# Kernel tuning notes

Measured on AMD Instinct MI355X. Metric: run time of the kernel, lower is better.

## Reference

```python
import jax, jax.numpy as jnp
import numpy as np
from jax.ops import segment_sum

N = 20000; IN = 256; HID = 256; Z = 64; DEC_H = 64; E = 120000; NEG = 5
BETA = 1.0; LN_EPS = 1e-5; TAU_MIN = 1e-4


def setup_inputs() -> dict:
    rng = np.random.default_rng(0)
    a = rng.integers(0, N, E)
    b = (a + 1 + rng.integers(0, N - 1, E)) % N  # guarantees a != b
    lo, hi = np.minimum(a, b), np.maximum(a, b)
    pos_edge = jnp.asarray(np.stack([lo, hi]), dtype=jnp.int32)          # [2,E], i<j single copy
    edge_index = jnp.asarray(np.stack([np.concatenate([lo, hi]),
                                       np.concatenate([hi, lo])]), dtype=jnp.int32)  # [2,2E] undirected
    neg_edge = jnp.asarray(rng.integers(0, N, (2, NEG * E)), dtype=jnp.int32)
    ks = jax.random.split(jax.random.key(0), 12)
    p = lambda i, shape, s=0.02: (jax.random.normal(ks[i], shape, jnp.float32) * s)
    return dict(
        x=p(0, (N, IN), 1.0), eps=p(1, (N, Z), 1.0),
        edge_index=edge_index, pos_edge=pos_edge, neg_edge=neg_edge,
        W1=p(2, (IN, HID)), b1=jnp.zeros((HID,), jnp.float32),
        g1=jnp.ones((HID,), jnp.float32), bt1=jnp.zeros((HID,), jnp.float32),
        Wmu=p(3, (HID, Z)), bmu=jnp.zeros((Z,), jnp.float32),
        Wlv=p(4, (HID, Z)), blv=jnp.zeros((Z,), jnp.float32),
        Wd1=p(5, (Z, Z)), bd1=jnp.zeros((Z,), jnp.float32),
        Wd2=p(6, (Z, Z)), bd2=jnp.zeros((Z,), jnp.float32),
        Wa=p(7, (4 * Z, DEC_H)), ba=jnp.zeros((DEC_H,), jnp.float32),
        Wb=p(8, (DEC_H, 1)), bb=jnp.zeros((1,), jnp.float32),
        tau=jnp.array(1.0, jnp.float32))


def _gcn_plain(h, src, dst, W, b):
    # GCNConv(add_self_loops=False, normalize=False): unnormalized scatter-add
    m = h @ W                                   # [N,F]
    return segment_sum(m[src], dst, num_segments=N) + b


def _gcn_norm(h, src, dst, W, b):
    # GCNConv defaults: self loops + symmetric normalization
    loops = jnp.arange(N, dtype=src.dtype)
    s = jnp.concatenate([src, loops]); d = jnp.concatenate([dst, loops])
    deg = segment_sum(jnp.ones_like(d, jnp.float32), d, num_segments=N)  # in-degree incl self
    dis = jax.lax.rsqrt(jnp.maximum(deg, 1.0))
    norm = dis[s] * dis[d]                      # [Emsg+N]
    m = h @ W
    return segment_sum(m[s] * norm[:, None], d, num_segments=N) + b


def _layernorm(h, g, bt):
    mu = jnp.mean(h, axis=-1, keepdims=True)
    var = jnp.mean((h - mu) ** 2, axis=-1, keepdims=True)
    return (h - mu) * jax.lax.rsqrt(var + LN_EPS) * g + bt


def _forward(x, eps, edge_index, pos_edge, neg_edge, W1, b1, g1, bt1, Wmu, bmu,
             Wlv, blv, Wd1, bd1, Wd2, bd2, Wa, ba, Wb, bb, tau):
    src, dst = edge_index[0], edge_index[1]
    # Encoder (dropout inactive: eval-mode reference)
    h1 = jax.nn.relu(_layernorm(_gcn_plain(x, src, dst, W1, b1), g1, bt1))
    mu = _gcn_plain(h1, src, dst, Wmu, bmu)
    logvar = _gcn_plain(h1, src, dst, Wlv, blv)
    z = mu + eps * jnp.exp(0.5 * logvar)
    # EdgeDecoder: 2 normalized GCN passes over positive (i<j) edges only
    ps, pd = pos_edge[0], pos_edge[1]
    h = jax.nn.relu(_gcn_norm(z, ps, pd, Wd1, bd1))
    h = jax.nn.relu(_gcn_norm(h, ps, pd, Wd2, bd2))
    # edge gather -> concat features -> MLP
    eu = jnp.concatenate([pos_edge[0], neg_edge[0]])
    ev = jnp.concatenate([pos_edge[1], neg_edge[1]])
    hu, hv = h[eu], h[ev]                        # [Ep+En, Z]
    phi = jnp.concatenate([hu, hv, jnp.abs(hu - hv), hu * hv], axis=-1)  # [Ep+En, 4Z]
    logits = (jax.nn.relu(phi @ Wa + ba) @ Wb + bb)[:, 0]
    logits = logits / jnp.clip(tau, TAU_MIN)
    # weighted BCE-with-logits; pos_weight = #neg/#pos = NEG
    n_pos = pos_edge.shape[1]; n_neg = neg_edge.shape[1]
    labels = jnp.concatenate([jnp.ones((n_pos,), jnp.float32), jnp.zeros((n_neg,), jnp.float32)])
    pw = jnp.float32(n_neg) / jnp.float32(n_pos)
    recon = -jnp.mean(pw * labels * jax.nn.log_sigmoid(logits)
                      + (1.0 - labels) * jax.nn.log_sigmoid(-logits))
    kl = -0.5 * jnp.mean(1.0 + logvar - mu ** 2 - jnp.exp(logvar))
    loss = recon + BETA * kl
    return loss, recon, kl


def reference(x, eps, edge_index, pos_edge, neg_edge, W1, b1, g1, bt1, Wmu, bmu,
              Wlv, blv, Wd1, bd1, Wd2, bd2, Wa, ba, Wb, bb, tau):
    return _forward(x, eps, edge_index, pos_edge, neg_edge, W1, b1, g1, bt1, Wmu,
                    bmu, Wlv, blv, Wd1, bd1, Wd2, bd2, Wa, ba, Wb, bb, tau)
```

## Files before the change

kernel.cpp:

```cpp
#include <hip/hip_runtime.h>
#include <hip/hip_bf16.h>
#include <math.h>

#define N_NODES 20000
#define E2      240000
#define EP      120000
#define ENEG    600000
#define ETOT    720000
#define NTILE   11250
#define EMLP_BLOCKS 1024

#define WA_B  64
#define W1T_B 256
#define WML_B 128
#define UV_B  2813
#define HA_B  938
#define HP_B  469
#define FA_B  938
#define FP_B  469
#define DIS_B 79

typedef __attribute__((ext_vector_type(8))) short bf16x8;
typedef __attribute__((ext_vector_type(4))) float f32x4;

__device__ __forceinline__ float logsigf(float x) {
    return fminf(x, 0.0f) - log1pf(expf(-fabsf(x)));
}

__device__ __forceinline__ unsigned short f2bf(float f) {
    unsigned u = __float_as_uint(f);
    u += 0x7FFF + ((u >> 16) & 1);
    return (unsigned short)(u >> 16);
}

__device__ __forceinline__ float bflo(unsigned u) { return __uint_as_float(u << 16); }
__device__ __forceinline__ float bfhi(unsigned u) { return __uint_as_float(u & 0xFFFF0000u); }

__device__ __forceinline__ void store_out(float v, float* p) { *p = v; }
__device__ __forceinline__ void store_out(float v, unsigned short* p) { *p = f2bf(v); }

__device__ __forceinline__ int4 pack_phi(unsigned hu, unsigned hv) {
    const float fu0 = __uint_as_float(hu << 16);
    const float fu1 = __uint_as_float(hu & 0xFFFF0000u);
    const float fv0 = __uint_as_float(hv << 16);
    const float fv1 = __uint_as_float(hv & 0xFFFF0000u);
    const float ad0 = fabsf(fu0 - fv0), ad1 = fabsf(fu1 - fv1);
    const float pr0 = fu0 * fv0,        pr1 = fu1 * fv1;
    union { __hip_bfloat162 h; int u; } c0, c1;
    c0.h = __float22bfloat162_rn(float2{ad0, pr0});
    c1.h = __float22bfloat162_rn(float2{ad1, pr1});
    int4 r;
    r.x = (int)((hu & 0xFFFFu) | (hv << 16));
    r.y = c0.u;
    r.z = (int)((hu >> 16) | (hv & 0xFFFF0000u));
    r.w = c1.u;
    return r;
}

__global__ void k_prep_csr(const float* __restrict__ Wa, unsigned short* __restrict__ WaT,
                           const float* __restrict__ W1, unsigned short* __restrict__ W1T,
                           const float* __restrict__ Wmu, const float* __restrict__ Wlv,
                           unsigned short* __restrict__ WmlT,
                           const int* __restrict__ pos, const int* __restrict__ neg,
                           int2* __restrict__ uv,
                           const int* __restrict__ e_dst, int* __restrict__ cntA,
                           const int* __restrict__ pd, int* __restrict__ cntP) {
    const int b = blockIdx.x, tid = threadIdx.x;
    if (b < WA_B) {
        const int idx = b * 256 + tid;
        const int n = idx >> 8, kp = idx & 255;
        const int d = kp >> 2, part = kp & 3;
        WaT[idx] = f2bf(Wa[(part * 64 + d) * 64 + n]);
    } else if (b < WA_B + W1T_B) {
        const int idx = (b - WA_B) * 256 + tid;
        const int n = idx >> 8, k = idx & 255;
        W1T[idx] = f2bf(W1[k * 256 + n]);
    } else if (b < WA_B + W1T_B + WML_B) {
        const int idx = (b - WA_B - W1T_B) * 256 + tid;
        const int n = idx >> 8, k = idx & 255;
        const float* W = (n & 1) ? Wlv : Wmu;
        WmlT[idx] = f2bf(W[k * 64 + (n >> 1)]);
    } else if (b < WA_B + W1T_B + WML_B + UV_B) {
        const int j = (b - WA_B - W1T_B - WML_B) * 256 + tid;
        if (j < ETOT) {
            int u, v;
            if (j < EP) { u = pos[j]; v = pos[EP + j]; }
            else        { u = neg[j - EP]; v = neg[ENEG + (j - EP)]; }
            uv[j] = make_int2(u, v);
        }
    } else if (b < WA_B + W1T_B + WML_B + UV_B + HA_B) {
        const int e = (b - WA_B - W1T_B - WML_B - UV_B) * 256 + tid;
        if (e < E2) atomicAdd(&cntA[e_dst[e]], 1);
    } else {
        const int e = (b - WA_B - W1T_B - WML_B - UV_B - HA_B) * 256 + tid;
        if (e < EP) atomicAdd(&cntP[pd[e]], 1);
    }
}

__global__ __launch_bounds__(1024) void k_scan2(int* __restrict__ cntA, int* __restrict__ rsA,
                                                int* __restrict__ cntP, int* __restrict__ rsP) {
    int* cnt = blockIdx.x ? cntP : cntA;
    int* rs  = blockIdx.x ? rsP  : rsA;
    int* cur = cnt;
    const int n = N_NODES;
    __shared__ int wexc[16];
    __shared__ int s_carry, s_tot;
    const int tid = threadIdx.x, lane = tid & 63, wid = tid >> 6;
    if (tid == 0) s_carry = 0;
    __syncthreads();
    for (int base = 0; base < n; base += 1024) {
        const int i = base + tid;
        const int v = (i < n) ? cnt[i] : 0;
        int x = v;
#pragma unroll
        for (int d = 1; d < 64; d <<= 1) {
            const int t = __shfl_up(x, d, 64);
            if (lane >= d) x += t;
        }
        if (lane == 63) wexc[wid] = x;
        __syncthreads();
        if (tid == 0) {
            int a = 0;
#pragma unroll
            for (int k = 0; k < 16; ++k) { const int t = wexc[k]; wexc[k] = a; a += t; }
            s_tot = a;
        }
        __syncthreads();
        const int excl = s_carry + wexc[wid] + x - v;
        if (i < n) { rs[i] = excl; cur[i] = excl; }
        __syncthreads();
        if (tid == 0) s_carry += s_tot;
        __syncthreads();
    }
    if (tid == 0) rs[n] = s_carry;
}

__global__ void k_finish_csr(const int* __restrict__ e_src, const int* __restrict__ e_dst,
                             int* __restrict__ curA, int* __restrict__ adjA,
                             const int* __restrict__ ps, const int* __restrict__ pd,
                             int* __restrict__ curP, int* __restrict__ adjP,
                             const int* __restrict__ rsP, float* __restrict__ dis) {
    const int b = blockIdx.x, tid = threadIdx.x;
    if (b < FA_B) {
        const int e = b * 256 + tid;
        if (e < E2) {
            const int p = atomicAdd(&curA[e_dst[e]], 1);
            adjA[p] = e_src[e];
        }
    } else if (b < FA_B + FP_B) {
        const int e = (b - FA_B) * 256 + tid;
        if (e < EP) {
            const int p = atomicAdd(&curP[pd[e]], 1);
            adjP[p] = ps[e];
        }
    } else {
        const int i = (b - FA_B - FP_B) * 256 + tid;
        if (i < N_NODES) dis[i] = rsqrtf((float)(rsP[i + 1] - rsP[i] + 1));
    }
}

__global__ __launch_bounds__(256) void k_mm_xW1_mfma(const float* __restrict__ x,
                                                     const unsigned short* __restrict__ W1T,
                                                     unsigned short* __restrict__ m1) {
    __shared__ unsigned short sA[32 * 264];
    const int tid = threadIdx.x;
    const int w = tid >> 6, lane = tid & 63;
    const int l15 = lane & 15, quad = lane >> 4;
    const int mb = blockIdx.x >> 2, nb = blockIdx.x & 3;

    for (int i = tid; i < 2048; i += 256) {
        const int row = i >> 6, kc = (i & 63) << 2;
        const float4 xv = *(const float4*)&x[((long)mb * 32 + row) * 256 + kc];
        union { unsigned short s[4]; unsigned long long ll; } pk;
        pk.s[0] = f2bf(xv.x); pk.s[1] = f2bf(xv.y);
        pk.s[2] = f2bf(xv.z); pk.s[3] = f2bf(xv.w);
        *(unsigned long long*)&sA[row * 264 + kc] = pk.ll;
    }

    bf16x8 breg[8];
#pragma unroll
    for (int ks = 0; ks < 8; ++ks)
        breg[ks] = *(const bf16x8*)&W1T[((nb * 64 + w * 16 + l15) << 8) + ks * 32 + quad * 8];
    __syncthreads();

    f32x4 acc[2];
    acc[0] = (f32x4){0.f,0.f,0.f,0.f};
    acc[1] = (f32x4){0.f,0.f,0.f,0.f};
#pragma unroll
    for (int ks = 0; ks < 8; ++ks) {
#pragma unroll
        for (int st = 0; st < 2; ++st) {
            const bf16x8 af = *(const bf16x8*)&sA[(st * 16 + l15) * 264 + ks * 32 + quad * 8];
            acc[st] = __builtin_amdgcn_mfma_f32_16x16x32_bf16(af, breg[ks], acc[st], 0, 0, 0);
        }
    }
#pragma unroll
    for (int st = 0; st < 2; ++st)
#pragma unroll
        for (int r = 0; r < 4; ++r)
            m1[((long)mb * 32 + st * 16 + quad * 4 + r) * 256 + nb * 64 + w * 16 + l15] =
                f2bf(acc[st][r]);
}

__global__ __launch_bounds__(256) void k_gather_ln(const unsigned short* __restrict__ m1,
                                                   const int* __restrict__ rs,
                                                   const int* __restrict__ adj,
                                                   const float* __restrict__ b1,
                                                   const float* __restrict__ g1,
                                                   const float* __restrict__ bt1,
                                                   unsigned short* __restrict__ h1) {
    const int wid = threadIdx.x >> 6, lane = threadIdx.x & 63;
    const int n = blockIdx.x * 4 + wid;
    const int beg = rs[n], end = rs[n + 1];
    float4 a0 = {0.f,0.f,0.f,0.f}, a1 = {0.f,0.f,0.f,0.f};
    int j = beg;
    for (; j + 1 < end; j += 2) {
        const int s0 = adj[j], s1 = adj[j + 1];
        const uint2 u = *(const uint2*)(m1 + (long)s0 * 256 + lane * 4);
        const uint2 v = *(const uint2*)(m1 + (long)s1 * 256 + lane * 4);
        a0.x += bflo(u.x); a0.y += bfhi(u.x); a0.z += bflo(u.y); a0.w += bfhi(u.y);
        a1.x += bflo(v.x); a1.y += bfhi(v.x); a1.z += bflo(v.y); a1.w += bfhi(v.y);
    }
    if (j < end) {
        const int s0 = adj[j];
        const uint2 u = *(const uint2*)(m1 + (long)s0 * 256 + lane * 4);
        a0.x += bflo(u.x); a0.y += bfhi(u.x); a0.z += bflo(u.y); a0.w += bfhi(u.y);
    }
    float4 v;
    const float4 b = *(const float4*)(b1 + lane * 4);
    v.x = a0.x + a1.x + b.x; v.y = a0.y + a1.y + b.y;
    v.z = a0.z + a1.z + b.z; v.w = a0.w + a1.w + b.w;
    float s  = v.x + v.y + v.z + v.w;
    float sq = v.x * v.x + v.y * v.y + v.z * v.z + v.w * v.w;
    for (int o = 32; o > 0; o >>= 1) {
        s  += __shfl_xor(s, o, 64);
        sq += __shfl_xor(sq, o, 64);
    }
    const float mean = s * (1.0f / 256.0f);
    const float var  = sq * (1.0f / 256.0f) - mean * mean;
    const float rsv = rsqrtf(var + 1e-5f);
    const float4 g  = *(const float4*)(g1 + lane * 4);
    const float4 bt = *(const float4*)(bt1 + lane * 4);
    union { unsigned short sh[4]; unsigned long long ll; } pk;
    pk.sh[0] = f2bf(fmaxf((v.x - mean) * rsv * g.x + bt.x, 0.f));
    pk.sh[1] = f2bf(fmaxf((v.y - mean) * rsv * g.y + bt.y, 0.f));
    pk.sh[2] = f2bf(fmaxf((v.z - mean) * rsv * g.z + bt.z, 0.f));
    pk.sh[3] = f2bf(fmaxf((v.w - mean) * rsv * g.w + bt.w, 0.f));
    *(unsigned long long*)&h1[(long)n * 256 + lane * 4] = pk.ll;
}

__global__ __launch_bounds__(256) void k_mm_hml_mfma(const unsigned short* __restrict__ h1,
                                                     const unsigned short* __restrict__ WmlT,
                                                     unsigned short* __restrict__ hml) {
    __shared__ unsigned short sA[32 * 264];
    const int tid = threadIdx.x;
    const int w = tid >> 6, lane = tid & 63;
    const int l15 = lane & 15, quad = lane >> 4;
    const int mb = blockIdx.x >> 1, nb = blockIdx.x & 1;

    for (int i = tid; i < 1024; i += 256) {
        const int row = i >> 5, kc = (i & 31) << 3;
        *(int4*)&sA[row * 264 + kc] = *(const int4*)&h1[((long)mb * 32 + row) * 256 + kc];
    }

    bf16x8 breg[8];
#pragma unroll
    for (int ks = 0; ks < 8; ++ks)
        breg[ks] = *(const bf16x8*)&WmlT[((nb * 64 + w * 16 + l15) << 8) + ks * 32 + quad * 8];
    __syncthreads();

    f32x4 acc[2];
    acc[0] = (f32x4){0.f,0.f,0.f,0.f};
    acc[1] = (f32x4){0.f,0.f,0.f,0.f};
#pragma unroll
    for (int ks = 0; ks < 8; ++ks) {
#pragma unroll
        for (int st = 0; st < 2; ++st) {
            const bf16x8 af = *(const bf16x8*)&sA[(st * 16 + l15) * 264 + ks * 32 + quad * 8];
            acc[st] = __builtin_amdgcn_mfma_f32_16x16x32_bf16(af, breg[ks], acc[st], 0, 0, 0);
        }
    }
#pragma unroll
    for (int st = 0; st < 2; ++st)
#pragma unroll
        for (int r = 0; r < 4; ++r)
            hml[((long)mb * 32 + st * 16 + quad * 4 + r) * 128 + nb * 64 + w * 16 + l15] =
                f2bf(acc[st][r]);
}

__global__ __launch_bounds__(256) void k_gather_mulv(const unsigned short* __restrict__ hml,
                                                     const int* __restrict__ rs,
                                                     const int* __restrict__ adj,
                                                     const float* __restrict__ bmu,
                                                     const float* __restrict__ blv,
                                                     const float* __restrict__ eps,
                                                     float* __restrict__ z,
                                                     double* __restrict__ kl_part) {
    __shared__ double sKL[4];
    const int wid = threadIdx.x >> 6, lane = threadIdx.x & 63;
    const int n = blockIdx.x * 4 + wid;
    const int beg = rs[n], end = rs[n + 1];
    float amu0 = 0.f, amu1 = 0.f, alv0 = 0.f, alv1 = 0.f;
    int j = beg;
    for (; j + 1 < end; j += 2) {
        const int s0 = adj[j], s1 = adj[j + 1];
        const unsigned u0 = *(const unsigned*)(hml + (long)s0 * 128 + lane * 2);
        const unsigned u1 = *(const unsigned*)(hml + (long)s1 * 128 + lane * 2);
        amu0 += bflo(u0); alv0 += bfhi(u0);
        amu1 += bflo(u1); alv1 += bfhi(u1);
    }
    if (j < end) {
        const int s0 = adj[j];
        const unsigned u0 = *(const unsigned*)(hml + (long)s0 * 128 + lane * 2);
        amu0 += bflo(u0); alv0 += bfhi(u0);
    }
    const float mu = amu0 + amu1 + bmu[lane];
    const float lv = alv0 + alv1 + blv[lane];
    z[(long)n * 64 + lane] = mu + eps[(long)n * 64 + lane] * expf(0.5f * lv);
    float term = 1.0f + lv - mu * mu - expf(lv);
    for (int o = 32; o > 0; o >>= 1) term += __shfl_xor(term, o, 64);
    if (lane == 0) sKL[wid] = (double)term;
    __syncthreads();
    if (threadIdx.x == 0)
        kl_part[blockIdx.x] = sKL[0] + sKL[1] + sKL[2] + sKL[3];
}

template <typename OUT>
__global__ __launch_bounds__(256) void k_dec_fused(const float* __restrict__ feat,
                                                   const int* __restrict__ rs,
                                                   const int* __restrict__ adj,
                                                   const float* __restrict__ dis,
                                                   const float* __restrict__ Wd,
                                                   const float* __restrict__ bd,
                                                   OUT* __restrict__ out) {
    __shared__ float sW[64 * 64];
    __shared__ float rows[4][64];
    const int tid = threadIdx.x;
    {
        const float4* w4 = (const float4*)Wd;
        float4* sw4 = (float4*)sW;
        for (int i = tid; i < 1024; i += 256) sw4[i] = w4[i];
    }
    const int wid = tid >> 6, lane = tid & 63;
    const int n = blockIdx.x * 4 + wid;
    const int beg = rs[n], end = rs[n + 1];
    float a0 = 0.f, a1 = 0.f;
    int j = beg;
    for (; j + 1 < end; j += 2) {
        const int s0 = adj[j], s1 = adj[j + 1];
        a0 += feat[(long)s0 * 64 + lane] * dis[s0];
        a1 += feat[(long)s1 * 64 + lane] * dis[s1];
    }
    if (j < end) {
        const int s0 = adj[j];
        a0 += feat[(long)s0 * 64 + lane] * dis[s0];
    }
    const float dn = dis[n];
    rows[wid][lane] = (a0 + a1) * dn + feat[(long)n * 64 + lane] * dn * dn;
    __syncthreads();
    float acc = 0.f;
    for (int k = 0; k < 64; k += 4) {
        const float4 a = *(const float4*)&rows[wid][k];
        acc += a.x * sW[(k+0)*64+lane] + a.y * sW[(k+1)*64+lane]
             + a.z * sW[(k+2)*64+lane] + a.w * sW[(k+3)*64+lane];
    }
    store_out(fmaxf(acc + bd[lane], 0.f), &out[(long)n * 64 + lane]);
}

__global__ __launch_bounds__(256, 4) void k_edge_mlp_mfma(
        const unsigned short* __restrict__ h2bf,
        const int2* __restrict__ uv,
        const unsigned short* __restrict__ WaT,
        const float* __restrict__ ba,
        const float* __restrict__ Wb,
        const float* __restrict__ bb,
        const float* __restrict__ tau,
        double* __restrict__ recon_part) {
    __shared__ unsigned short sPhi[64 * 264];
    __shared__ float sEp[256];
    __shared__ double sRed[4];
    const int tid = threadIdx.x;
    const int w = tid >> 6, lane = tid & 63;
    const int l15 = lane & 15, quad = lane >> 4;
    const int ge = lane >> 3;
    const int c  = lane & 7;

    bf16x8 breg[8];
#pragma unroll
    for (int ks = 0; ks < 8; ++ks)
        breg[ks] = *(const bf16x8*)&WaT[(w * 16 + l15) * 256 + ks * 32 + quad * 8];

    const float4 ba4 = *(const float4*)&ba[w * 16 + quad * 4];
    const float4 wb4 = *(const float4*)&Wb[w * 16 + quad * 4];
    const float bb0 = bb[0];
    const float itau = 1.0f / fmaxf(tau[0], 1e-4f);

    float lsum = 0.f;

    int t = blockIdx.x;
    int2 uv0 = uv[(long)t * 64 + w * 16 + ge];
    int2 uv1 = uv[(long)t * 64 + w * 16 + 8 + ge];
    int4 hu0 = *(const int4*)&h2bf[(long)uv0.x * 64 + c * 8];
    int4 hv0 = *(const int4*)&h2bf[(long)uv0.y * 64 + c * 8];
    int4 hu1 = *(const int4*)&h2bf[(long)uv1.x * 64 + c * 8];
    int4 hv1 = *(const int4*)&h2bf[(long)uv1.y * 64 + c * 8];

    for (; t < NTILE; t += EMLP_BLOCKS) {
        {
            unsigned short* d0 = &sPhi[(w * 16 + ge) * 264 + c * 32];
            *(int4*)(d0 +  0) = pack_phi((unsigned)hu0.x, (unsigned)hv0.x);
            *(int4*)(d0 +  8) = pack_phi((unsigned)hu0.y, (unsigned)hv0.y);
            *(int4*)(d0 + 16) = pack_phi((unsigned)hu0.z, (unsigned)hv0.z);
            *(int4*)(d0 + 24) = pack_phi((unsigned)hu0.w, (unsigned)hv0.w);
            unsigned short* d1 = &sPhi[(w * 16 + 8 + ge) * 264 + c * 32];
            *(int4*)(d1 +  0) = pack_phi((unsigned)hu1.x, (unsigned)hv1.x);
            *(int4*)(d1 +  8) = pack_phi((unsigned)hu1.y, (unsigned)hv1.y);
            *(int4*)(d1 + 16) = pack_phi((unsigned)hu1.z, (unsigned)hv1.z);
            *(int4*)(d1 + 24) = pack_phi((unsigned)hu1.w, (unsigned)hv1.w);
        }
        __syncthreads();

        const int tn = t + EMLP_BLOCKS;
        if (tn < NTILE) {
            uv0 = uv[(long)tn * 64 + w * 16 + ge];
            uv1 = uv[(long)tn * 64 + w * 16 + 8 + ge];
            hu0 = *(const int4*)&h2bf[(long)uv0.x * 64 + c * 8];
            hv0 = *(const int4*)&h2bf[(long)uv0.y * 64 + c * 8];
            hu1 = *(const int4*)&h2bf[(long)uv1.x * 64 + c * 8];
            hv1 = *(const int4*)&h2bf[(long)uv1.y * 64 + c * 8];
        }

        f32x4 acc[4];
#pragma unroll
        for (int mt = 0; mt < 4; ++mt) acc[mt] = (f32x4){0.f, 0.f, 0.f, 0.f};
#pragma unroll
        for (int ks = 0; ks < 8; ++ks) {
#pragma unroll
            for (int mt = 0; mt < 4; ++mt) {
                const bf16x8 bf = *(const bf16x8*)&sPhi[(mt * 16 + l15) * 264 +
                                                        ks * 32 + quad * 8];
                acc[mt] = __builtin_amdgcn_mfma_f32_16x16x32_bf16(breg[ks], bf, acc[mt], 0, 0, 0);
            }
        }

        float sv[4];
#pragma unroll
        for (int mt = 0; mt < 4; ++mt) {
            float s = fmaxf(acc[mt][0] + ba4.x, 0.f) * wb4.x
                    + fmaxf(acc[mt][1] + ba4.y, 0.f) * wb4.y
                    + fmaxf(acc[mt][2] + ba4.z, 0.f) * wb4.z
                    + fmaxf(acc[mt][3] + ba4.w, 0.f) * wb4.w;
            s += __shfl_xor(s, 16, 64);
            s += __shfl_xor(s, 32, 64);
            sv[mt] = s;
        }
        const float ssel = (quad == 0) ? sv[0] : (quad == 1) ? sv[1]
                         : (quad == 2) ? sv[2] : sv[3];
        sEp[(w << 6) + lane] = ssel;
        __syncthreads();

        if (lane < 16) {
            const int et = (w << 4) + lane;
            const float s_e = sEp[et] + sEp[64 + et] + sEp[128 + et] + sEp[192 + et];
            const long j = (long)t * 64 + et;
            const float logit = (s_e + bb0) * itau;
            lsum += (j < EP) ? 5.0f * logsigf(logit) : logsigf(-logit);
        }
    }

    for (int o = 32; o > 0; o >>= 1) lsum += __shfl_xor(lsum, o, 64);
    if (lane == 0) sRed[w] = (double)lsum;
    __syncthreads();
    if (tid == 0)
        recon_part[blockIdx.x] = sRed[0] + sRed[1] + sRed[2] + sRed[3];
}

__global__ __launch_bounds__(1024) void k_final(const double* __restrict__ kl_part,
                                                const double* __restrict__ recon_part,
                                                float* __restrict__ out) {
    __shared__ double sK[16], sR[16];
    const int tid = threadIdx.x, lane = tid & 63, wid = tid >> 6;
    double kl = 0.0, rc = 0.0;
    for (int i = tid; i < 5000; i += 1024) kl += kl_part[i];
    for (int i = tid; i < EMLP_BLOCKS; i += 1024) rc += recon_part[i];
    for (int o = 32; o > 0; o >>= 1) {
        kl += __shfl_xor(kl, o, 64);
        rc += __shfl_xor(rc, o, 64);
    }
    if (lane == 0) { sK[wid] = kl; sR[wid] = rc; }
    __syncthreads();
    if (tid == 0) {
        double K = 0.0, R = 0.0;
        for (int i = 0; i < 16; ++i) { K += sK[i]; R += sR[i]; }
        const double recon = -R / (double)ETOT;
        const double klv = -0.5 * K / ((double)N_NODES * 64.0);
        out[0] = (float)(recon + klv);
        out[1] = (float)recon;
        out[2] = (float)klv;
    }
}

extern "C" void kernel_launch(void* const* d_in, const int* in_sizes, int n_in,
                              void* d_out, int out_size, void* d_ws, size_t ws_size,
                              hipStream_t stream) {
    const float* x   = (const float*)d_in[0];
    const float* eps = (const float*)d_in[1];
    const int* EI    = (const int*)d_in[2];
    const int* pos   = (const int*)d_in[3];
    const int* neg   = (const int*)d_in[4];
    const float* W1  = (const float*)d_in[5];
    const float* b1  = (const float*)d_in[6];
    const float* g1  = (const float*)d_in[7];
    const float* bt1 = (const float*)d_in[8];
    const float* Wmu = (const float*)d_in[9];
    const float* bmu = (const float*)d_in[10];
    const float* Wlv = (const float*)d_in[11];
    const float* blv = (const float*)d_in[12];
    const float* Wd1 = (const float*)d_in[13];
    const float* bd1 = (const float*)d_in[14];
    const float* Wd2 = (const float*)d_in[15];
    const float* bd2 = (const float*)d_in[16];
    const float* Wa  = (const float*)d_in[17];
    const float* ba  = (const float*)d_in[18];
    const float* Wb  = (const float*)d_in[19];
    const float* bb  = (const float*)d_in[20];
    const float* tau = (const float*)d_in[21];

    const int* e_src = EI;
    const int* e_dst = EI + E2;
    const int* ps = pos;
    const int* pd = pos + EP;

    float* ws = (float*)d_ws;
    unsigned short* m1bf  = (unsigned short*)ws;
    unsigned short* hmlbf = (unsigned short*)ws;
    float* hdec  = ws + 2560000;
    unsigned short* h2bf = (unsigned short*)(ws + 3840000);
    unsigned short* h1bf = (unsigned short*)(ws + 5120000);
    float* z     = ws + 10240000;
    float* dis   = ws + 11520000;
    unsigned short* WaT = (unsigned short*)(ws + 11540004);
    int* cntA = (int*)(ws + 11548200);
    int* rsA  = (int*)(ws + 11568200);
    int* adjA = (int*)(ws + 11588204);
    int* cntP = (int*)(ws + 11828204);
    int* rsP  = (int*)(ws + 11848204);
    int* adjP = (int*)(ws + 11868208);
    int2* uv  = (int2*)(ws + 11988208);
    double* kl_part    = (double*)(ws + 13428208);
    double* recon_part = (double*)(ws + 13438208);
    unsigned short* W1T  = (unsigned short*)(ws + 13440256);
    unsigned short* WmlT = (unsigned short*)(ws + 13473024);

    hipMemsetAsync(cntA, 0, N_NODES * 4, stream);
    hipMemsetAsync(cntP, 0, N_NODES * 4, stream);

    k_prep_csr<<<WA_B + W1T_B + WML_B + UV_B + HA_B + HP_B, 256, 0, stream>>>(
        Wa, WaT, W1, W1T, Wmu, Wlv, WmlT, pos, neg, uv, e_dst, cntA, pd, cntP);
    k_scan2<<<2, 1024, 0, stream>>>(cntA, rsA, cntP, rsP);
    k_finish_csr<<<FA_B + FP_B + DIS_B, 256, 0, stream>>>(
        e_src, e_dst, cntA, adjA, ps, pd, cntP, adjP, rsP, dis);

    k_mm_xW1_mfma<<<2500, 256, 0, stream>>>(x, W1T, m1bf);
    k_gather_ln<<<5000, 256, 0, stream>>>(m1bf, rsA, adjA, b1, g1, bt1, h1bf);
    k_mm_hml_mfma<<<1250, 256, 0, stream>>>(h1bf, WmlT, hmlbf);
    k_gather_mulv<<<5000, 256, 0, stream>>>(hmlbf, rsA, adjA, bmu, blv, eps, z, kl_part);

    k_dec_fused<float><<<5000, 256, 0, stream>>>(z, rsP, adjP, dis, Wd1, bd1, hdec);
    k_dec_fused<unsigned short><<<5000, 256, 0, stream>>>(hdec, rsP, adjP, dis, Wd2, bd2, h2bf);

    k_edge_mlp_mfma<<<EMLP_BLOCKS, 256, 0, stream>>>(h2bf, uv, WaT, ba, Wb, bb, tau, recon_part);
    k_final<<<1, 1024, 0, stream>>>(kl_part, recon_part, (float*)d_out);
}
```

Measured before the change: 353.1 us.

## Store decoder intermediates in bf16 and retile edge-MLP MFMA as 2x2 per wave

The latent z and the first decoder hidden layer are now stored as bf16 instead of fp32, which halves the bytes moved by the neighbor gathers in both decoder kernels. The edge-MLP kernel changes its wave split from one 16-column N slice over all 64 edges to a 2x2 (edge half × column half) layout. Each wave now reuses each phi fragment loaded from LDS for two MFMAs, which cuts LDS reads, at the cost of twice as many weight registers. Rounding z and the decoder hidden layer to bf16 adds precision loss.

Result: no change. 358.1 us (+1.4%).

```diff
diff --git a/kernel.cpp b/kernel.cpp
--- a/kernel.cpp
+++ b/kernel.cpp
@@ -38,6 +38,10 @@
 
 __device__ __forceinline__ void store_out(float v, float* p) { *p = v; }
 __device__ __forceinline__ void store_out(float v, unsigned short* p) { *p = f2bf(v); }
+__device__ __forceinline__ float load_in(const float* p) { return *p; }
+__device__ __forceinline__ float load_in(const unsigned short* p) {
+    return __uint_as_float(((unsigned)*p) << 16);
+}
 
 __device__ __forceinline__ int4 pack_phi(unsigned hu, unsigned hv) {
     const float fu0 = __uint_as_float(hu << 16);
@@ -294,7 +298,7 @@
                                                      const float* __restrict__ bmu,
                                                      const float* __restrict__ blv,
                                                      const float* __restrict__ eps,
-                                                     float* __restrict__ z,
+                                                     unsigned short* __restrict__ z,
                                                      double* __restrict__ kl_part) {
     __shared__ double sKL[4];
     const int wid = threadIdx.x >> 6, lane = threadIdx.x & 63;
@@ -316,7 +320,7 @@
     }
     const float mu = amu0 + amu1 + bmu[lane];
     const float lv = alv0 + alv1 + blv[lane];
-    z[(long)n * 64 + lane] = mu + eps[(long)n * 64 + lane] * expf(0.5f * lv);
+    z[(long)n * 64 + lane] = f2bf(mu + eps[(long)n * 64 + lane] * expf(0.5f * lv));
     float term = 1.0f + lv - mu * mu - expf(lv);
     for (int o = 32; o > 0; o >>= 1) term += __shfl_xor(term, o, 64);
     if (lane == 0) sKL[wid] = (double)term;
@@ -325,8 +329,8 @@
         kl_part[blockIdx.x] = sKL[0] + sKL[1] + sKL[2] + sKL[3];
 }
 
-template <typename OUT>
-__global__ __launch_bounds__(256) void k_dec_fused(const float* __restrict__ feat,
+template <typename IN, typename OUT>
+__global__ __launch_bounds__(256) void k_dec_fused(const IN* __restrict__ feat,
                                                    const int* __restrict__ rs,
                                                    const int* __restrict__ adj,
                                                    const float* __restrict__ dis,
@@ -348,15 +352,15 @@
     int j = beg;
     for (; j + 1 < end; j += 2) {
         const int s0 = adj[j], s1 = adj[j + 1];
-        a0 += feat[(long)s0 * 64 + lane] * dis[s0];
-        a1 += feat[(long)s1 * 64 + lane] * dis[s1];
+        a0 += load_in(&feat[(long)s0 * 64 + lane]) * dis[s0];
+        a1 += load_in(&feat[(long)s1 * 64 + lane]) * dis[s1];
     }
     if (j < end) {
         const int s0 = adj[j];
-        a0 += feat[(long)s0 * 64 + lane] * dis[s0];
+        a0 += load_in(&feat[(long)s0 * 64 + lane]) * dis[s0];
     }
     const float dn = dis[n];
-    rows[wid][lane] = (a0 + a1) * dn + feat[(long)n * 64 + lane] * dn * dn;
+    rows[wid][lane] = (a0 + a1) * dn + load_in(&feat[(long)n * 64 + lane]) * dn * dn;
     __syncthreads();
     float acc = 0.f;
     for (int k = 0; k < 64; k += 4) {
@@ -377,21 +381,30 @@
         const float* __restrict__ tau,
         double* __restrict__ recon_part) {
     __shared__ unsigned short sPhi[64 * 264];
-    __shared__ float sEp[256];
+    __shared__ float sEp[128];
     __shared__ double sRed[4];
     const int tid = threadIdx.x;
     const int w = tid >> 6, lane = tid & 63;
     const int l15 = lane & 15, quad = lane >> 4;
     const int ge = lane >> 3;
     const int c  = lane & 7;
-
-    bf16x8 breg[8];
-#pragma unroll
-    for (int ks = 0; ks < 8; ++ks)
-        breg[ks] = *(const bf16x8*)&WaT[(w * 16 + l15) * 256 + ks * 32 + quad * 8];
-
-    const float4 ba4 = *(const float4*)&ba[w * 16 + quad * 4];
-    const float4 wb4 = *(const float4*)&Wb[w * 16 + quad * 4];
+    const int eh = w & 1;
+    const int nh = w >> 1;
+
+    bf16x8 breg[2][8];
+#pragma unroll
+    for (int nt = 0; nt < 2; ++nt)
+#pragma unroll
+        for (int ks = 0; ks < 8; ++ks)
+            breg[nt][ks] = *(const bf16x8*)&WaT[(nh * 32 + nt * 16 + l15) * 256 +
+                                                ks * 32 + quad * 8];
+
+    float4 ba4[2], wb4[2];
+#pragma unroll
+    for (int nt = 0; nt < 2; ++nt) {
+        ba4[nt] = *(const float4*)&ba[nh * 32 + nt * 16 + quad * 4];
+        wb4[nt] = *(const float4*)&Wb[nh * 32 + nt * 16 + quad * 4];
+    }
     const float bb0 = bb[0];
     const float itau = 1.0f / fmaxf(tau[0], 1e-4f);
 
@@ -430,39 +443,46 @@
             hv1 = *(const int4*)&h2bf[(long)uv1.y * 64 + c * 8];
         }
 
-        f32x4 acc[4];
-#pragma unroll
-        for (int mt = 0; mt < 4; ++mt) acc[mt] = (f32x4){0.f, 0.f, 0.f, 0.f};
+        f32x4 acc[2][2];
+#pragma unroll
+        for (int mt = 0; mt < 2; ++mt)
+#pragma unroll
+            for (int nt = 0; nt < 2; ++nt) acc[mt][nt] = (f32x4){0.f, 0.f, 0.f, 0.f};
 #pragma unroll
         for (int ks = 0; ks < 8; ++ks) {
 #pragma unroll
-            for (int mt = 0; mt < 4; ++mt) {
-                const bf16x8 bf = *(const bf16x8*)&sPhi[(mt * 16 + l15) * 264 +
+            for (int mt = 0; mt < 2; ++mt) {
+                const bf16x8 bf = *(const bf16x8*)&sPhi[(eh * 32 + mt * 16 + l15) * 264 +
                                                         ks * 32 + quad * 8];
-                acc[mt] = __builtin_amdgcn_mfma_f32_16x16x32_bf16(breg[ks], bf, acc[mt], 0, 0, 0);
+#pragma unroll
+                for (int nt = 0; nt < 2; ++nt)
+                    acc[mt][nt] = __builtin_amdgcn_mfma_f32_16x16x32_bf16(
+                        breg[nt][ks], bf, acc[mt][nt], 0, 0, 0);
             }
         }
 
-        float sv[4];
-#pragma unroll
-        for (int mt = 0; mt < 4; ++mt) {
-            float s = fmaxf(acc[mt][0] + ba4.x, 0.f) * wb4.x
-                    + fmaxf(acc[mt][1] + ba4.y, 0.f) * wb4.y
-                    + fmaxf(acc[mt][2] + ba4.z, 0.f) * wb4.z
-                    + fmaxf(acc[mt][3] + ba4.w, 0.f) * wb4.w;
+        float sv[2];
+#pragma unroll
+        for (int mt = 0; mt < 2; ++mt) {
+            float s = 0.f;
+#pragma unroll
+            for (int nt = 0; nt < 2; ++nt)
+                s += fmaxf(acc[mt][nt][0] + ba4[nt].x, 0.f) * wb4[nt].x
+                   + fmaxf(acc[mt][nt][1] + ba4[nt].y, 0.f) * wb4[nt].y
+                   + fmaxf(acc[mt][nt][2] + ba4[nt].z, 0.f) * wb4[nt].z
+                   + fmaxf(acc[mt][nt][3] + ba4[nt].w, 0.f) * wb4[nt].w;
             s += __shfl_xor(s, 16, 64);
             s += __shfl_xor(s, 32, 64);
             sv[mt] = s;
         }
-        const float ssel = (quad == 0) ? sv[0] : (quad == 1) ? sv[1]
-                         : (quad == 2) ? sv[2] : sv[3];
-        sEp[(w << 6) + lane] = ssel;
+        if (lane < 32) sEp[w * 32 + lane] = (lane & 16) ? sv[1] : sv[0];
         __syncthreads();
 
         if (lane < 16) {
-            const int et = (w << 4) + lane;
-            const float s_e = sEp[et] + sEp[64 + et] + sEp[128 + et] + sEp[192 + et];
-            const long j = (long)t * 64 + et;
+            const int e = w * 16 + lane;
+            const int h = e >> 5, e31 = e & 31;
+            const float s_e = sEp[h * 32 + e31] + sEp[(h + 2) * 32 + e31];
+            const long j = (long)t * 64 + e;
             const float logit = (s_e + bb0) * itau;
             lsum += (j < EP) ? 5.0f * logsigf(logit) : logsigf(-logit);
         }
@@ -534,10 +554,10 @@
     float* ws = (float*)d_ws;
     unsigned short* m1bf  = (unsigned short*)ws;
     unsigned short* hmlbf = (unsigned short*)ws;
-    float* hdec  = ws + 2560000;
+    unsigned short* hdec  = (unsigned short*)(ws + 2560000);
     unsigned short* h2bf = (unsigned short*)(ws + 3840000);
     unsigned short* h1bf = (unsigned short*)(ws + 5120000);
-    float* z     = ws + 10240000;
+    unsigned short* z    = (unsigned short*)(ws + 10240000);
     float* dis   = ws + 11520000;
     unsigned short* WaT = (unsigned short*)(ws + 11540004);
     int* cntA = (int*)(ws + 11548200);
@@ -566,8 +586,10 @@
     k_mm_hml_mfma<<<1250, 256, 0, stream>>>(h1bf, WmlT, hmlbf);
     k_gather_mulv<<<5000, 256, 0, stream>>>(hmlbf, rsA, adjA, bmu, blv, eps, z, kl_part);
 
-    k_dec_fused<float><<<5000, 256, 0, stream>>>(z, rsP, adjP, dis, Wd1, bd1, hdec);
-    k_dec_fused<unsigned short><<<5000, 256, 0, stream>>>(hdec, rsP, adjP, dis, Wd2, bd2, h2bf);
+    k_dec_fused<unsigned short, unsigned short><<<5000, 256, 0, stream>>>(
+        z, rsP, adjP, dis, Wd1, bd1, hdec);
+    k_dec_fused<unsigned short, unsigned short><<<5000, 256, 0, stream>>>(
+        hdec, rsP, adjP, dis, Wd2, bd2, h2bf);
 
     k_edge_mlp_mfma<<<EMLP_BLOCKS, 256, 0, stream>>>(h2bf, uv, WaT, ba, Wb, bb, tau, recon_part);
     k_final<<<1, 1024, 0, stream>>>(kl_part, recon_part, (float*)d_out);
```
